# Performance work log

Hardware: AMD Instinct MI355X
Metric: run time of the kernel (lower is better)

Reference implementation:

```python
import jax, jax.numpy as jnp
import numpy as np

B, T, K, H, HID, OUT = 128, 128, 8, 3, 256, 2
LOG_STD_MIN, LOG_STD_MAX = -20.0, 2.0


def setup_inputs() -> dict:
    key = jax.random.key(0)
    ks = jax.random.split(key, 12)
    def lin(k, fan_in, fan_out, scale=0.05):
        return jax.random.normal(k, (fan_in, fan_out), dtype=jnp.float32) * scale
    return {
        "state": jax.random.normal(ks[0], (B, T, K), dtype=jnp.float32),
        "noise": jax.random.normal(ks[1], (B, T, OUT), dtype=jnp.float32),
        "Wq": lin(ks[2], K, H * K),
        "Wk": lin(ks[3], K, H * K),
        "Wv": lin(ks[4], K, H * K),
        "W1": lin(ks[5], H * K + K, HID),
        "b1": jnp.zeros((HID,), jnp.float32),
        "W2": lin(ks[6], HID, HID),
        "b2": jnp.zeros((HID,), jnp.float32),
        "Wmu": jax.random.uniform(ks[7], (HID, OUT), jnp.float32, -0.003, 0.003),
        "bmu": jax.random.uniform(ks[8], (OUT,), jnp.float32, -0.003, 0.003),
        "Wls": jax.random.uniform(ks[9], (HID, OUT), jnp.float32, -0.003, 0.003),
        "bls": jax.random.uniform(ks[10], (OUT,), jnp.float32, -0.003, 0.003),
    }


def reference(state, noise, Wq, Wk, Wv, W1, b1, W2, b2, Wmu, bmu, Wls, bls):
    b, t, k = state.shape
    h = H
    # off-diagonal gather indices: idx[i, m] = m if m < i else m + 1  (j != i, ascending)
    cols = jnp.arange(t - 1)
    idx = cols[None, :] + (cols[None, :] >= jnp.arange(t)[:, None]).astype(jnp.int32)  # [t, t-1]
    # rel_state[b, i, m] = state[b, idx[i, m]] - state[b, i]   -> [b, t, t-1, k]
    rel = state[:, idx, :] - state[:, :, None, :]
    # per-head projections (no bias)
    q = (state @ Wq).reshape(b, t, h, k)                      # [b, t, h, k]
    keys = (rel @ Wk).reshape(b, t, t - 1, h, k)              # [b, t, t-1, h, k]
    vals = (rel @ Wv).reshape(b, t, t - 1, h, k)
    # each query attends over its own t-1 relative keys
    scores = jnp.einsum("bthk,btmhk->bhtm", q, keys) / jnp.sqrt(jnp.float32(k))
    w = jax.nn.softmax(scores, axis=-1)                       # [b, h, t, t-1]
    x = jnp.einsum("bhtm,btmhk->bthk", w, vals).reshape(b, t, h * k)
    x = jnp.concatenate([x, state], axis=-1)                  # [b, t, h*k + k]
    x = jax.nn.relu(x @ W1 + b1)
    x = jax.nn.relu(x @ W2 + b2)
    mu = jnp.tanh(x @ Wmu + bmu)
    log_std = jnp.tanh(x @ Wls + bls)
    log_std = LOG_STD_MIN + 0.5 * (LOG_STD_MAX - LOG_STD_MIN) * (log_std + 1.0)
    std = jnp.exp(log_std)
    z = mu + std * noise                                      # rsample
    action = jnp.tanh(z)
    half_log_2pi = jnp.float32(0.5 * np.log(2.0 * np.pi))
    normal_lp = -0.5 * noise * noise - log_std - half_log_2pi
    log_prob = normal_lp - jnp.log(1.0 - action * action + 1e-7)
    log_prob = jnp.sum(log_prob, axis=-1, keepdims=True)
    return action, log_prob
```

## Files before the change

### kernel.cpp

```cpp
#include <hip/hip_runtime.h>
#include <math.h>

namespace {
constexpr int B_  = 128;
constexpr int T_  = 128;
constexpr int K_  = 8;
constexpr int H_  = 3;
constexpr int HK_ = 24;
constexpr int HID_ = 256;
constexpr int OUT_ = 2;
constexpr int AW_  = 32;
}

typedef __attribute__((ext_vector_type(8))) short bf16x8;
typedef __attribute__((ext_vector_type(4))) float f32x4;

__device__ inline unsigned short f2bf(float x) {
    unsigned int u = __float_as_uint(x);
    u += 0x7FFFu + ((u >> 16) & 1u);
    return (unsigned short)(u >> 16);
}
__device__ inline float bflo(unsigned int u) { return __uint_as_float(u << 16); }
__device__ inline float bfhi(unsigned int u) { return __uint_as_float(u & 0xFFFF0000u); }

__global__ __launch_bounds__(256) void prep_kernel(
    const float* __restrict__ W1, const float* __restrict__ W2,
    unsigned short* __restrict__ w1t, unsigned short* __restrict__ w2t)
{
    int idx = blockIdx.x * 256 + threadIdx.x;
    if (idx < 65536) {
        int k = idx >> 8, n = idx & 255;
        w2t[n * 256 + k] = f2bf(W2[idx]);
    } else {
        int r = idx - 65536;
        int k = r >> 8, n = r & 255;
        w1t[n * 32 + k] = f2bf(W1[r]);
    }
}

__global__ __launch_bounds__(256) void fused_actor_kernel(
    const float* __restrict__ state,
    const float* __restrict__ noise,
    const float* __restrict__ Wq, const float* __restrict__ Wk,
    const float* __restrict__ Wv,
    const unsigned short* __restrict__ w1t, const float* __restrict__ b1,
    const unsigned short* __restrict__ w2t, const float* __restrict__ b2,
    const float* __restrict__ Wmu, const float* __restrict__ bmu,
    const float* __restrict__ Wls, const float* __restrict__ bls,
    float* __restrict__ out)
{
    __shared__ alignas(16) float st[T_][K_];
    __shared__ float wq_s[K_*HK_], wk_s[K_*HK_], wv_s[K_*HK_];
    __shared__ alignas(16) float Qs[32][HK_];
    __shared__ alignas(16) unsigned short Kb[H_][T_][8];
    __shared__ alignas(16) unsigned short Vb[H_][T_][8];
    __shared__ alignas(16) unsigned short a0b[32][40];
    __shared__ alignas(16) unsigned short x1s[32][264];
    __shared__ alignas(16) float Whs[HID_][4];
    __shared__ alignas(16) float hp[4][32][4];

    const int tid = threadIdx.x;
    const int b   = blockIdx.x >> 2;
    const int iq  = blockIdx.x & 3;

    ((float4*)&st[0][0])[tid] = ((const float4*)(state + (size_t)b*T_*K_))[tid];
    if (tid < K_*HK_) { wq_s[tid]=Wq[tid]; wk_s[tid]=Wk[tid]; wv_s[tid]=Wv[tid]; }
    Whs[tid][0] = Wmu[tid*OUT_+0]; Whs[tid][1] = Wmu[tid*OUT_+1];
    Whs[tid][2] = Wls[tid*OUT_+0]; Whs[tid][3] = Wls[tid*OUT_+1];
    __syncthreads();

    #pragma unroll
    for (int it = 0; it < 12; ++it) {
        int idx = it*256 + tid;
        int j = idx / HK_, col = idx % HK_;
        int h = col >> 3, k = col & 7;
        float ak = 0.f, av = 0.f;
        #pragma unroll
        for (int m = 0; m < K_; ++m) {
            float sv = st[j][m];
            ak = fmaf(sv, wk_s[m*HK_+col], ak);
            av = fmaf(sv, wv_s[m*HK_+col], av);
        }
        Kb[h][j][k] = f2bf(ak);
        Vb[h][j][k] = f2bf(av);
    }
    #pragma unroll
    for (int it = 0; it < 3; ++it) {
        int idx = it*256 + tid;
        int il = idx / HK_, col = idx % HK_;
        float aq = 0.f;
        #pragma unroll
        for (int m = 0; m < K_; ++m)
            aq = fmaf(st[iq*32+il][m], wq_s[m*HK_+col], aq);
        Qs[il][col] = aq * 0.35355339059327373f;
    }
    __syncthreads();

    const int w    = tid >> 6;
    const int lane = tid & 63;

    {
        const int i_sub = lane >> 3, jg = lane & 7;
        #pragma unroll
        for (int p = 0; p < 3; ++p) {
            const int pair = w*3 + p;
            const int h  = pair >> 2;
            const int ig = pair & 3;
            const int il = ig*8 + i_sub;
            const int iglob = iq*32 + il;
            const float4 q0 = *(const float4*)&Qs[il][h*8];
            const float4 q1 = *(const float4*)&Qs[il][h*8+4];
            float l = 0.f;
            float acc[8] = {0.f,0.f,0.f,0.f,0.f,0.f,0.f,0.f};
            #pragma unroll 4
            for (int t = 0; t < 16; ++t) {
                const int j = t*8 + jg;
                const int4 kk = *(const int4*)&Kb[h][j][0];
                float s;
                s = q0.x * bflo(kk.x) + q0.y * bfhi(kk.x)
                  + q0.z * bflo(kk.y) + q0.w * bfhi(kk.y)
                  + q1.x * bflo(kk.z) + q1.y * bfhi(kk.z)
                  + q1.z * bflo(kk.w) + q1.w * bfhi(kk.w);
                const float e = (j == iglob) ? 0.f : __expf(s);
                l += e;
                const int4 vv = *(const int4*)&Vb[h][j][0];
                acc[0] = fmaf(e, bflo(vv.x), acc[0]);
                acc[1] = fmaf(e, bfhi(vv.x), acc[1]);
                acc[2] = fmaf(e, bflo(vv.y), acc[2]);
                acc[3] = fmaf(e, bfhi(vv.y), acc[3]);
                acc[4] = fmaf(e, bflo(vv.z), acc[4]);
                acc[5] = fmaf(e, bfhi(vv.z), acc[5]);
                acc[6] = fmaf(e, bflo(vv.w), acc[6]);
                acc[7] = fmaf(e, bfhi(vv.w), acc[7]);
            }
            #pragma unroll
            for (int off = 1; off <= 4; off <<= 1) {
                l += __shfl_xor(l, off, 64);
                #pragma unroll
                for (int k = 0; k < 8; ++k) acc[k] += __shfl_xor(acc[k], off, 64);
            }
            if (jg == 0) {
                const float rl = 1.f / l;
                const int4 vi = *(const int4*)&Vb[h][iglob][0];
                float vs[8] = { bflo(vi.x), bfhi(vi.x), bflo(vi.y), bfhi(vi.y),
                                bflo(vi.z), bfhi(vi.z), bflo(vi.w), bfhi(vi.w) };
                unsigned int r01 = (unsigned int)f2bf(acc[0]*rl - vs[0])
                                 | ((unsigned int)f2bf(acc[1]*rl - vs[1]) << 16);
                unsigned int r23 = (unsigned int)f2bf(acc[2]*rl - vs[2])
                                 | ((unsigned int)f2bf(acc[3]*rl - vs[3]) << 16);
                unsigned int r45 = (unsigned int)f2bf(acc[4]*rl - vs[4])
                                 | ((unsigned int)f2bf(acc[5]*rl - vs[5]) << 16);
                unsigned int r67 = (unsigned int)f2bf(acc[6]*rl - vs[6])
                                 | ((unsigned int)f2bf(acc[7]*rl - vs[7]) << 16);
                int4 rr; rr.x = r01; rr.y = r23; rr.z = r45; rr.w = r67;
                *(int4*)&a0b[il][h*8] = rr;
            }
        }
    }
    {
        int il = tid >> 3, k = tid & 7;
        a0b[il][HK_ + k] = f2bf(st[iq*32 + il][k]);
    }
    __syncthreads();

    const int lq = (tid >> 4) & 3;
    const int ln = tid & 15;

    {
        bf16x8 a0 = *(const bf16x8*)&a0b[ln][lq*8];
        bf16x8 a1 = *(const bf16x8*)&a0b[16+ln][lq*8];
        #pragma unroll
        for (int nt = 0; nt < 4; ++nt) {
            const int n0 = (w*4 + nt)*16;
            bf16x8 bf = *(const bf16x8*)(w1t + (size_t)(n0+ln)*32 + lq*8);
            const float bias = b1[n0+ln];
            f32x4 c = {bias, bias, bias, bias};
            f32x4 d0 = __builtin_amdgcn_mfma_f32_16x16x32_bf16(a0, bf, c, 0, 0, 0);
            f32x4 d1 = __builtin_amdgcn_mfma_f32_16x16x32_bf16(a1, bf, c, 0, 0, 0);
            #pragma unroll
            for (int r = 0; r < 4; ++r) {
                x1s[lq*4 + r][n0+ln]      = f2bf(fmaxf(d0[r], 0.f));
                x1s[16 + lq*4 + r][n0+ln] = f2bf(fmaxf(d1[r], 0.f));
            }
        }
    }
    __syncthreads();

    f32x4 acc2[2][4];
    #pragma unroll
    for (int nt = 0; nt < 4; ++nt) {
        const float bias = b2[(w*4+nt)*16 + ln];
        f32x4 c = {bias, bias, bias, bias};
        acc2[0][nt] = c; acc2[1][nt] = c;
    }
    #pragma unroll 2
    for (int ks = 0; ks < 8; ++ks) {
        const int k0 = ks*32;
        bf16x8 a0 = *(const bf16x8*)&x1s[ln][k0 + lq*8];
        bf16x8 a1 = *(const bf16x8*)&x1s[16+ln][k0 + lq*8];
        #pragma unroll
        for (int nt = 0; nt < 4; ++nt) {
            bf16x8 bf = *(const bf16x8*)(w2t + (size_t)((w*4+nt)*16+ln)*256 + k0 + lq*8);
            acc2[0][nt] = __builtin_amdgcn_mfma_f32_16x16x32_bf16(a0, bf, acc2[0][nt], 0,0,0);
            acc2[1][nt] = __builtin_amdgcn_mfma_f32_16x16x32_bf16(a1, bf, acc2[1][nt], 0,0,0);
        }
    }

    {
        float p[2][4][4];
        #pragma unroll
        for (int mt = 0; mt < 2; ++mt)
            #pragma unroll
            for (int r = 0; r < 4; ++r)
                #pragma unroll
                for (int o = 0; o < 4; ++o) p[mt][r][o] = 0.f;
        #pragma unroll
        for (int nt = 0; nt < 4; ++nt) {
            const int n = (w*4+nt)*16 + ln;
            const f32x4 wh = *(const f32x4*)&Whs[n][0];
            #pragma unroll
            for (int mt = 0; mt < 2; ++mt) {
                #pragma unroll
                for (int r = 0; r < 4; ++r) {
                    const float x2 = fmaxf(acc2[mt][nt][r], 0.f);
                    p[mt][r][0] = fmaf(x2, wh[0], p[mt][r][0]);
                    p[mt][r][1] = fmaf(x2, wh[1], p[mt][r][1]);
                    p[mt][r][2] = fmaf(x2, wh[2], p[mt][r][2]);
                    p[mt][r][3] = fmaf(x2, wh[3], p[mt][r][3]);
                }
            }
        }
        #pragma unroll
        for (int off = 1; off <= 8; off <<= 1)
            #pragma unroll
            for (int mt = 0; mt < 2; ++mt)
                #pragma unroll
                for (int r = 0; r < 4; ++r)
                    #pragma unroll
                    for (int o = 0; o < 4; ++o)
                        p[mt][r][o] += __shfl_xor(p[mt][r][o], off, 64);
        if (ln == 0) {
            #pragma unroll
            for (int mt = 0; mt < 2; ++mt)
                #pragma unroll
                for (int r = 0; r < 4; ++r) {
                    f32x4 pv = {p[mt][r][0], p[mt][r][1], p[mt][r][2], p[mt][r][3]};
                    *(f32x4*)&hp[w][mt*16 + lq*4 + r][0] = pv;
                }
        }
    }
    __syncthreads();

    if (tid < 32) {
        const int r = tid;
        const int grow = b*T_ + iq*32 + r;
        float pre[4];
        #pragma unroll
        for (int o = 0; o < 4; ++o)
            pre[o] = hp[0][r][o] + hp[1][r][o] + hp[2][r][o] + hp[3][r][o];
        float lp = 0.f;
        #pragma unroll
        for (int o = 0; o < OUT_; ++o) {
            float mu  = tanhf(pre[o]   + bmu[o]);
            float lsp = tanhf(pre[2+o] + bls[o]);
            float log_std = -20.f + 11.f * (lsp + 1.f);
            float sd = __expf(log_std);
            float n  = noise[(size_t)grow*OUT_ + o];
            float z  = fmaf(sd, n, mu);
            float a  = tanhf(z);
            out[(size_t)grow*OUT_ + o] = a;
            lp += -0.5f*n*n - log_std - 0.91893853320467274f
                  - logf(1.f - a*a + 1e-7f);
        }
        out[(size_t)B_*T_*OUT_ + grow] = lp;
    }
}

extern "C" void kernel_launch(void* const* d_in, const int* in_sizes, int n_in,
                              void* d_out, int out_size, void* d_ws, size_t ws_size,
                              hipStream_t stream)
{
    const float* state = (const float*)d_in[0];
    const float* noise = (const float*)d_in[1];
    const float* Wq  = (const float*)d_in[2];
    const float* Wk  = (const float*)d_in[3];
    const float* Wv  = (const float*)d_in[4];
    const float* W1  = (const float*)d_in[5];
    const float* b1  = (const float*)d_in[6];
    const float* W2  = (const float*)d_in[7];
    const float* b2  = (const float*)d_in[8];
    const float* Wmu = (const float*)d_in[9];
    const float* bmu = (const float*)d_in[10];
    const float* Wls = (const float*)d_in[11];
    const float* bls = (const float*)d_in[12];
    float* out = (float*)d_out;

    unsigned short* w1t = (unsigned short*)d_ws;
    unsigned short* w2t = w1t + 8192;

    prep_kernel<<<dim3(288), dim3(256), 0, stream>>>(W1, W2, w1t, w2t);
    fused_actor_kernel<<<dim3(B_*4), dim3(256), 0, stream>>>(
        state, noise, Wq, Wk, Wv, w1t, b1, w2t, b2, Wmu, bmu, Wls, bls, out);
}
```

Measured before the change: 101.7 us.

## Halve rows per block to double grid size and vectorize weight prep

Each block now handles 16 query rows instead of 32, so the grid doubles to 1024 blocks and the attention loop uses 16 lanes per row with shorter trip counts. The MLP stage keeps one MFMA row tile per wave. The K/V projection is restructured so each thread computes a full key row and writes it with a vector store. The prep kernel now writes packed 8-element bf16 vectors per thread. The trade-off is that K/V projection and weight loads are repeated across twice as many blocks.

```diff
diff --git a/kernel.cpp b/kernel.cpp
--- a/kernel.cpp
+++ b/kernel.cpp
@@ -9,7 +9,6 @@
 constexpr int HK_ = 24;
 constexpr int HID_ = 256;
 constexpr int OUT_ = 2;
-constexpr int AW_  = 32;
 }
 
 typedef __attribute__((ext_vector_type(8))) short bf16x8;
@@ -27,14 +26,18 @@
     const float* __restrict__ W1, const float* __restrict__ W2,
     unsigned short* __restrict__ w1t, unsigned short* __restrict__ w2t)
 {
-    int idx = blockIdx.x * 256 + threadIdx.x;
-    if (idx < 65536) {
-        int k = idx >> 8, n = idx & 255;
-        w2t[n * 256 + k] = f2bf(W2[idx]);
+    const int n = threadIdx.x;
+    unsigned short tmp[8];
+    if (blockIdx.x < 32) {
+        const int k0 = blockIdx.x * 8;
+        #pragma unroll
+        for (int i = 0; i < 8; ++i) tmp[i] = f2bf(W2[(size_t)(k0+i)*HID_ + n]);
+        *(bf16x8*)(w2t + (size_t)n*256 + k0) = *(const bf16x8*)tmp;
     } else {
-        int r = idx - 65536;
-        int k = r >> 8, n = r & 255;
-        w1t[n * 32 + k] = f2bf(W1[r]);
+        const int k0 = (blockIdx.x - 32) * 8;
+        #pragma unroll
+        for (int i = 0; i < 8; ++i) tmp[i] = f2bf(W1[(size_t)(k0+i)*HID_ + n]);
+        *(bf16x8*)(w1t + (size_t)n*32 + k0) = *(const bf16x8*)tmp;
     }
 }
 
@@ -51,48 +54,61 @@
 {
     __shared__ alignas(16) float st[T_][K_];
     __shared__ float wq_s[K_*HK_], wk_s[K_*HK_], wv_s[K_*HK_];
-    __shared__ alignas(16) float Qs[32][HK_];
+    __shared__ alignas(16) float Qs[16][HK_];
     __shared__ alignas(16) unsigned short Kb[H_][T_][8];
     __shared__ alignas(16) unsigned short Vb[H_][T_][8];
-    __shared__ alignas(16) unsigned short a0b[32][40];
-    __shared__ alignas(16) unsigned short x1s[32][264];
+    __shared__ alignas(16) unsigned short a0b[16][40];
+    __shared__ alignas(16) unsigned short x1s[16][264];
     __shared__ alignas(16) float Whs[HID_][4];
-    __shared__ alignas(16) float hp[4][32][4];
+    __shared__ alignas(16) float hp[4][16][4];
 
     const int tid = threadIdx.x;
-    const int b   = blockIdx.x >> 2;
-    const int iq  = blockIdx.x & 3;
+    const int b   = blockIdx.x >> 3;
+    const int iq  = blockIdx.x & 7;
 
     ((float4*)&st[0][0])[tid] = ((const float4*)(state + (size_t)b*T_*K_))[tid];
     if (tid < K_*HK_) { wq_s[tid]=Wq[tid]; wk_s[tid]=Wk[tid]; wv_s[tid]=Wv[tid]; }
-    Whs[tid][0] = Wmu[tid*OUT_+0]; Whs[tid][1] = Wmu[tid*OUT_+1];
-    Whs[tid][2] = Wls[tid*OUT_+0]; Whs[tid][3] = Wls[tid*OUT_+1];
-    __syncthreads();
-
-    #pragma unroll
-    for (int it = 0; it < 12; ++it) {
-        int idx = it*256 + tid;
-        int j = idx / HK_, col = idx % HK_;
-        int h = col >> 3, k = col & 7;
-        float ak = 0.f, av = 0.f;
-        #pragma unroll
-        for (int m = 0; m < K_; ++m) {
-            float sv = st[j][m];
-            ak = fmaf(sv, wk_s[m*HK_+col], ak);
-            av = fmaf(sv, wv_s[m*HK_+col], av);
-        }
-        Kb[h][j][k] = f2bf(ak);
-        Vb[h][j][k] = f2bf(av);
-    }
-    #pragma unroll
-    for (int it = 0; it < 3; ++it) {
-        int idx = it*256 + tid;
-        int il = idx / HK_, col = idx % HK_;
-        float aq = 0.f;
-        #pragma unroll
-        for (int m = 0; m < K_; ++m)
-            aq = fmaf(st[iq*32+il][m], wq_s[m*HK_+col], aq);
-        Qs[il][col] = aq * 0.35355339059327373f;
+    { f32x4 wh = { Wmu[tid*OUT_+0], Wmu[tid*OUT_+1], Wls[tid*OUT_+0], Wls[tid*OUT_+1] };
+      *(f32x4*)&Whs[tid][0] = wh; }
+    __syncthreads();
+
+    if (tid < 128) {
+        const int j = tid;
+        const float4 s0 = *(const float4*)(state + (size_t)b*T_*K_ + j*8);
+        const float4 s1 = *(const float4*)(state + (size_t)b*T_*K_ + j*8 + 4);
+        const float sv[8] = {s0.x,s0.y,s0.z,s0.w,s1.x,s1.y,s1.z,s1.w};
+        #pragma unroll
+        for (int h = 0; h < H_; ++h) {
+            unsigned short kp[8], vp[8];
+            #pragma unroll
+            for (int k = 0; k < 8; ++k) {
+                const int col = h*8 + k;
+                float ak = 0.f, av = 0.f;
+                #pragma unroll
+                for (int m = 0; m < K_; ++m) {
+                    ak = fmaf(sv[m], wk_s[m*HK_+col], ak);
+                    av = fmaf(sv[m], wv_s[m*HK_+col], av);
+                }
+                kp[k] = f2bf(ak); vp[k] = f2bf(av);
+            }
+            *(bf16x8*)&Kb[h][j][0] = *(const bf16x8*)kp;
+            *(bf16x8*)&Vb[h][j][0] = *(const bf16x8*)vp;
+        }
+    } else {
+        const int t2 = tid - 128;
+        const int il = t2 >> 3;
+        const int c0 = (t2 & 7) * 3;
+        const float4 s0 = *(const float4*)&st[iq*16 + il][0];
+        const float4 s1 = *(const float4*)&st[iq*16 + il][4];
+        const float sv[8] = {s0.x,s0.y,s0.z,s0.w,s1.x,s1.y,s1.z,s1.w};
+        #pragma unroll
+        for (int cc = 0; cc < 3; ++cc) {
+            const int col = c0 + cc;
+            float aq = 0.f;
+            #pragma unroll
+            for (int m = 0; m < K_; ++m) aq = fmaf(sv[m], wq_s[m*HK_+col], aq);
+            Qs[il][col] = aq * 0.35355339059327373f;
+        }
     }
     __syncthreads();
 
@@ -100,21 +116,21 @@
     const int lane = tid & 63;
 
     {
-        const int i_sub = lane >> 3, jg = lane & 7;
+        const int i_sub = lane >> 4, jg = lane & 15;
         #pragma unroll
         for (int p = 0; p < 3; ++p) {
-            const int pair = w*3 + p;
-            const int h  = pair >> 2;
-            const int ig = pair & 3;
-            const int il = ig*8 + i_sub;
-            const int iglob = iq*32 + il;
+            const int pp = w*3 + p;
+            const int h  = pp >> 2;
+            const int ig = pp & 3;
+            const int il = ig*4 + i_sub;
+            const int iglob = iq*16 + il;
             const float4 q0 = *(const float4*)&Qs[il][h*8];
             const float4 q1 = *(const float4*)&Qs[il][h*8+4];
             float l = 0.f;
             float acc[8] = {0.f,0.f,0.f,0.f,0.f,0.f,0.f,0.f};
-            #pragma unroll 4
-            for (int t = 0; t < 16; ++t) {
-                const int j = t*8 + jg;
+            #pragma unroll
+            for (int t = 0; t < 8; ++t) {
+                const int j = t*16 + jg;
                 const int4 kk = *(const int4*)&Kb[h][j][0];
                 float s;
                 s = q0.x * bflo(kk.x) + q0.y * bfhi(kk.x)
@@ -134,7 +150,7 @@
                 acc[7] = fmaf(e, bfhi(vv.w), acc[7]);
             }
             #pragma unroll
-            for (int off = 1; off <= 4; off <<= 1) {
+            for (int off = 1; off <= 8; off <<= 1) {
                 l += __shfl_xor(l, off, 64);
                 #pragma unroll
                 for (int k = 0; k < 8; ++k) acc[k] += __shfl_xor(acc[k], off, 64);
@@ -142,8 +158,8 @@
             if (jg == 0) {
                 const float rl = 1.f / l;
                 const int4 vi = *(const int4*)&Vb[h][iglob][0];
-                float vs[8] = { bflo(vi.x), bfhi(vi.x), bflo(vi.y), bfhi(vi.y),
-                                bflo(vi.z), bfhi(vi.z), bflo(vi.w), bfhi(vi.w) };
+                const float vs[8] = { bflo(vi.x), bfhi(vi.x), bflo(vi.y), bfhi(vi.y),
+                                      bflo(vi.z), bfhi(vi.z), bflo(vi.w), bfhi(vi.w) };
                 unsigned int r01 = (unsigned int)f2bf(acc[0]*rl - vs[0])
                                  | ((unsigned int)f2bf(acc[1]*rl - vs[1]) << 16);
                 unsigned int r23 = (unsigned int)f2bf(acc[2]*rl - vs[2])
@@ -157,9 +173,9 @@
             }
         }
     }
-    {
-        int il = tid >> 3, k = tid & 7;
-        a0b[il][HK_ + k] = f2bf(st[iq*32 + il][k]);
+    if (tid < 128) {
+        const int il = tid >> 3, k = tid & 7;
+        a0b[il][HK_ + k] = f2bf(st[iq*16 + il][k]);
     }
     __syncthreads();
 
@@ -167,93 +183,78 @@
     const int ln = tid & 15;
 
     {
-        bf16x8 a0 = *(const bf16x8*)&a0b[ln][lq*8];
-        bf16x8 a1 = *(const bf16x8*)&a0b[16+ln][lq*8];
+        const bf16x8 a0 = *(const bf16x8*)&a0b[ln][lq*8];
         #pragma unroll
         for (int nt = 0; nt < 4; ++nt) {
             const int n0 = (w*4 + nt)*16;
-            bf16x8 bf = *(const bf16x8*)(w1t + (size_t)(n0+ln)*32 + lq*8);
+            const bf16x8 bf = *(const bf16x8*)(w1t + (size_t)(n0+ln)*32 + lq*8);
             const float bias = b1[n0+ln];
             f32x4 c = {bias, bias, bias, bias};
-            f32x4 d0 = __builtin_amdgcn_mfma_f32_16x16x32_bf16(a0, bf, c, 0, 0, 0);
-            f32x4 d1 = __builtin_amdgcn_mfma_f32_16x16x32_bf16(a1, bf, c, 0, 0, 0);
-            #pragma unroll
-            for (int r = 0; r < 4; ++r) {
-                x1s[lq*4 + r][n0+ln]      = f2bf(fmaxf(d0[r], 0.f));
-                x1s[16 + lq*4 + r][n0+ln] = f2bf(fmaxf(d1[r], 0.f));
-            }
-        }
-    }
-    __syncthreads();
-
-    f32x4 acc2[2][4];
+            f32x4 d = __builtin_amdgcn_mfma_f32_16x16x32_bf16(a0, bf, c, 0, 0, 0);
+            #pragma unroll
+            for (int r = 0; r < 4; ++r)
+                x1s[lq*4 + r][n0+ln] = f2bf(fmaxf(d[r], 0.f));
+        }
+    }
+    __syncthreads();
+
+    f32x4 acc2[4];
     #pragma unroll
     for (int nt = 0; nt < 4; ++nt) {
         const float bias = b2[(w*4+nt)*16 + ln];
         f32x4 c = {bias, bias, bias, bias};
-        acc2[0][nt] = c; acc2[1][nt] = c;
+        acc2[nt] = c;
     }
     #pragma unroll 2
     for (int ks = 0; ks < 8; ++ks) {
         const int k0 = ks*32;
-        bf16x8 a0 = *(const bf16x8*)&x1s[ln][k0 + lq*8];
-        bf16x8 a1 = *(const bf16x8*)&x1s[16+ln][k0 + lq*8];
+        const bf16x8 a0 = *(const bf16x8*)&x1s[ln][k0 + lq*8];
         #pragma unroll
         for (int nt = 0; nt < 4; ++nt) {
-            bf16x8 bf = *(const bf16x8*)(w2t + (size_t)((w*4+nt)*16+ln)*256 + k0 + lq*8);
-            acc2[0][nt] = __builtin_amdgcn_mfma_f32_16x16x32_bf16(a0, bf, acc2[0][nt], 0,0,0);
-            acc2[1][nt] = __builtin_amdgcn_mfma_f32_16x16x32_bf16(a1, bf, acc2[1][nt], 0,0,0);
+            const bf16x8 bf = *(const bf16x8*)(w2t + (size_t)((w*4+nt)*16+ln)*256 + k0 + lq*8);
+            acc2[nt] = __builtin_amdgcn_mfma_f32_16x16x32_bf16(a0, bf, acc2[nt], 0, 0, 0);
         }
     }
 
     {
-        float p[2][4][4];
-        #pragma unroll
-        for (int mt = 0; mt < 2; ++mt)
-            #pragma unroll
-            for (int r = 0; r < 4; ++r)
-                #pragma unroll
-                for (int o = 0; o < 4; ++o) p[mt][r][o] = 0.f;
+        float p[4][4];
+        #pragma unroll
+        for (int r = 0; r < 4; ++r)
+            #pragma unroll
+            for (int o = 0; o < 4; ++o) p[r][o] = 0.f;
         #pragma unroll
         for (int nt = 0; nt < 4; ++nt) {
             const int n = (w*4+nt)*16 + ln;
             const f32x4 wh = *(const f32x4*)&Whs[n][0];
             #pragma unroll
-            for (int mt = 0; mt < 2; ++mt) {
+            for (int r = 0; r < 4; ++r) {
+                const float x2 = fmaxf(acc2[nt][r], 0.f);
+                p[r][0] = fmaf(x2, wh[0], p[r][0]);
+                p[r][1] = fmaf(x2, wh[1], p[r][1]);
+                p[r][2] = fmaf(x2, wh[2], p[r][2]);
+                p[r][3] = fmaf(x2, wh[3], p[r][3]);
+            }
+        }
+        #pragma unroll
+        for (int off = 1; off <= 8; off <<= 1)
+            #pragma unroll
+            for (int r = 0; r < 4; ++r)
                 #pragma unroll
-                for (int r = 0; r < 4; ++r) {
-                    const float x2 = fmaxf(acc2[mt][nt][r], 0.f);
-                    p[mt][r][0] = fmaf(x2, wh[0], p[mt][r][0]);
-                    p[mt][r][1] = fmaf(x2, wh[1], p[mt][r][1]);
-                    p[mt][r][2] = fmaf(x2, wh[2], p[mt][r][2]);
-                    p[mt][r][3] = fmaf(x2, wh[3], p[mt][r][3]);
-                }
-            }
-        }
-        #pragma unroll
-        for (int off = 1; off <= 8; off <<= 1)
-            #pragma unroll
-            for (int mt = 0; mt < 2; ++mt)
-                #pragma unroll
-                for (int r = 0; r < 4; ++r)
-                    #pragma unroll
-                    for (int o = 0; o < 4; ++o)
-                        p[mt][r][o] += __shfl_xor(p[mt][r][o], off, 64);
+                for (int o = 0; o < 4; ++o)
+                    p[r][o] += __shfl_xor(p[r][o], off, 64);
         if (ln == 0) {
             #pragma unroll
-            for (int mt = 0; mt < 2; ++mt)
-                #pragma unroll
-                for (int r = 0; r < 4; ++r) {
-                    f32x4 pv = {p[mt][r][0], p[mt][r][1], p[mt][r][2], p[mt][r][3]};
-                    *(f32x4*)&hp[w][mt*16 + lq*4 + r][0] = pv;
-                }
-        }
-    }
-    __syncthreads();
-
-    if (tid < 32) {
+            for (int r = 0; r < 4; ++r) {
+                f32x4 pv = {p[r][0], p[r][1], p[r][2], p[r][3]};
+                *(f32x4*)&hp[w][lq*4 + r][0] = pv;
+            }
+        }
+    }
+    __syncthreads();
+
+    if (tid < 16) {
         const int r = tid;
-        const int grow = b*T_ + iq*32 + r;
+        const int grow = b*T_ + iq*16 + r;
         float pre[4];
         #pragma unroll
         for (int o = 0; o < 4; ++o)
@@ -298,7 +299,7 @@
     unsigned short* w1t = (unsigned short*)d_ws;
     unsigned short* w2t = w1t + 8192;
 
-    prep_kernel<<<dim3(288), dim3(256), 0, stream>>>(W1, W2, w1t, w2t);
-    fused_actor_kernel<<<dim3(B_*4), dim3(256), 0, stream>>>(
+    prep_kernel<<<dim3(36), dim3(256), 0, stream>>>(W1, W2, w1t, w2t);
+    fused_actor_kernel<<<dim3(B_*8), dim3(256), 0, stream>>>(
         state, noise, Wq, Wk, Wv, w1t, b1, w2t, b2, Wmu, bmu, Wls, bls, out);
 }
```

Measured after the change: 111.5 us. +9.7%, slower.

## Precompute Q/K/V projections once per batch in prep kernel and use DPP reductions

Applied to the files above, without the earlier changes.

Moves the K/V/Q projections out of the fused kernel into the prep kernel, so they are computed once per batch instead of once per quarter-block (4x redundant before). The results are stored to global workspace in bf16/fp32, and the attention loop reads them from global/L2 rather than LDS. Cross-lane shuffle reductions are replaced by DPP-based adds, and the prep kernel's weight transposes now use vectorized stores. The risk is extra global traffic and the attention inner loop hitting L2 instead of LDS.

```diff
diff --git a/kernel.cpp b/kernel.cpp
--- a/kernel.cpp
+++ b/kernel.cpp
@@ -9,7 +9,6 @@
 constexpr int HK_ = 24;
 constexpr int HID_ = 256;
 constexpr int OUT_ = 2;
-constexpr int AW_  = 32;
 }
 
 typedef __attribute__((ext_vector_type(8))) short bf16x8;
@@ -23,79 +22,115 @@
 __device__ inline float bflo(unsigned int u) { return __uint_as_float(u << 16); }
 __device__ inline float bfhi(unsigned int u) { return __uint_as_float(u & 0xFFFF0000u); }
 
+template <int CTRL>
+__device__ inline float dpp_add(float v) {
+    int t = __builtin_amdgcn_update_dpp(0, __float_as_int(v), CTRL, 0xF, 0xF, true);
+    return v + __int_as_float(t);
+}
+__device__ inline float red8(float v) {
+    v = dpp_add<0xB1>(v); v = dpp_add<0x4E>(v); return dpp_add<0x141>(v);
+}
+__device__ inline float red16(float v) {
+    return dpp_add<0x140>(red8(v));
+}
+
 __global__ __launch_bounds__(256) void prep_kernel(
+    const float* __restrict__ state,
+    const float* __restrict__ Wq, const float* __restrict__ Wk,
+    const float* __restrict__ Wv,
     const float* __restrict__ W1, const float* __restrict__ W2,
-    unsigned short* __restrict__ w1t, unsigned short* __restrict__ w2t)
+    unsigned short* __restrict__ w1t, unsigned short* __restrict__ w2t,
+    unsigned short* __restrict__ kb, unsigned short* __restrict__ vb,
+    float* __restrict__ qsc)
 {
-    int idx = blockIdx.x * 256 + threadIdx.x;
-    if (idx < 65536) {
-        int k = idx >> 8, n = idx & 255;
-        w2t[n * 256 + k] = f2bf(W2[idx]);
+    __shared__ float wq_s[K_*HK_], wk_s[K_*HK_], wv_s[K_*HK_];
+    const int tid = threadIdx.x;
+    const int blk = blockIdx.x;
+
+    if (blk < 32) {
+        const int k0 = blk * 8;
+        unsigned short tmp[8];
+        #pragma unroll
+        for (int i = 0; i < 8; ++i) tmp[i] = f2bf(W2[(size_t)(k0+i)*HID_ + tid]);
+        *(bf16x8*)(w2t + (size_t)tid*256 + k0) = *(const bf16x8*)tmp;
+        return;
+    }
+    if (blk < 36) {
+        const int k0 = (blk - 32) * 8;
+        unsigned short tmp[8];
+        #pragma unroll
+        for (int i = 0; i < 8; ++i) tmp[i] = f2bf(W1[(size_t)(k0+i)*HID_ + tid]);
+        *(bf16x8*)(w1t + (size_t)tid*32 + k0) = *(const bf16x8*)tmp;
+        return;
+    }
+
+    const int b = blk - 36;
+    if (tid < K_*HK_) { wq_s[tid]=Wq[tid]; wk_s[tid]=Wk[tid]; wv_s[tid]=Wv[tid]; }
+    __syncthreads();
+
+    const float* sb = state + (size_t)b*T_*K_;
+    if (tid < 128) {
+        const int j = tid;
+        const float4 s0 = *(const float4*)(sb + j*8);
+        const float4 s1 = *(const float4*)(sb + j*8 + 4);
+        const float sv[8] = {s0.x,s0.y,s0.z,s0.w,s1.x,s1.y,s1.z,s1.w};
+        #pragma unroll
+        for (int h = 0; h < H_; ++h) {
+            unsigned short kp[8], vp[8];
+            #pragma unroll
+            for (int k = 0; k < 8; ++k) {
+                const int col = h*8 + k;
+                float ak = 0.f, av = 0.f;
+                #pragma unroll
+                for (int m = 0; m < K_; ++m) {
+                    ak = fmaf(sv[m], wk_s[m*HK_+col], ak);
+                    av = fmaf(sv[m], wv_s[m*HK_+col], av);
+                }
+                kp[k] = f2bf(ak); vp[k] = f2bf(av);
+            }
+            const size_t off = ((size_t)(b*H_ + h)*T_ + j) * 8;
+            *(bf16x8*)(kb + off) = *(const bf16x8*)kp;
+            *(bf16x8*)(vb + off) = *(const bf16x8*)vp;
+        }
     } else {
-        int r = idx - 65536;
-        int k = r >> 8, n = r & 255;
-        w1t[n * 32 + k] = f2bf(W1[r]);
+        const int i = tid - 128;
+        const float4 s0 = *(const float4*)(sb + i*8);
+        const float4 s1 = *(const float4*)(sb + i*8 + 4);
+        const float sv[8] = {s0.x,s0.y,s0.z,s0.w,s1.x,s1.y,s1.z,s1.w};
+        float q[HK_];
+        #pragma unroll
+        for (int col = 0; col < HK_; ++col) {
+            float aq = 0.f;
+            #pragma unroll
+            for (int m = 0; m < K_; ++m) aq = fmaf(sv[m], wq_s[m*HK_+col], aq);
+            q[col] = aq * 0.35355339059327373f;
+        }
+        float* qo = qsc + (size_t)(b*T_ + i)*HK_;
+        #pragma unroll
+        for (int c = 0; c < 6; ++c)
+            *(float4*)(qo + c*4) = *(const float4*)&q[c*4];
     }
 }
 
 __global__ __launch_bounds__(256) void fused_actor_kernel(
     const float* __restrict__ state,
     const float* __restrict__ noise,
-    const float* __restrict__ Wq, const float* __restrict__ Wk,
-    const float* __restrict__ Wv,
+    const unsigned short* __restrict__ kb, const unsigned short* __restrict__ vb,
+    const float* __restrict__ qsc,
     const unsigned short* __restrict__ w1t, const float* __restrict__ b1,
     const unsigned short* __restrict__ w2t, const float* __restrict__ b2,
     const float* __restrict__ Wmu, const float* __restrict__ bmu,
     const float* __restrict__ Wls, const float* __restrict__ bls,
     float* __restrict__ out)
 {
-    __shared__ alignas(16) float st[T_][K_];
-    __shared__ float wq_s[K_*HK_], wk_s[K_*HK_], wv_s[K_*HK_];
-    __shared__ alignas(16) float Qs[32][HK_];
-    __shared__ alignas(16) unsigned short Kb[H_][T_][8];
-    __shared__ alignas(16) unsigned short Vb[H_][T_][8];
     __shared__ alignas(16) unsigned short a0b[32][40];
     __shared__ alignas(16) unsigned short x1s[32][264];
-    __shared__ alignas(16) float Whs[HID_][4];
     __shared__ alignas(16) float hp[4][32][4];
 
-    const int tid = threadIdx.x;
-    const int b   = blockIdx.x >> 2;
-    const int iq  = blockIdx.x & 3;
-
-    ((float4*)&st[0][0])[tid] = ((const float4*)(state + (size_t)b*T_*K_))[tid];
-    if (tid < K_*HK_) { wq_s[tid]=Wq[tid]; wk_s[tid]=Wk[tid]; wv_s[tid]=Wv[tid]; }
-    Whs[tid][0] = Wmu[tid*OUT_+0]; Whs[tid][1] = Wmu[tid*OUT_+1];
-    Whs[tid][2] = Wls[tid*OUT_+0]; Whs[tid][3] = Wls[tid*OUT_+1];
-    __syncthreads();
-
-    #pragma unroll
-    for (int it = 0; it < 12; ++it) {
-        int idx = it*256 + tid;
-        int j = idx / HK_, col = idx % HK_;
-        int h = col >> 3, k = col & 7;
-        float ak = 0.f, av = 0.f;
-        #pragma unroll
-        for (int m = 0; m < K_; ++m) {
-            float sv = st[j][m];
-            ak = fmaf(sv, wk_s[m*HK_+col], ak);
-            av = fmaf(sv, wv_s[m*HK_+col], av);
-        }
-        Kb[h][j][k] = f2bf(ak);
-        Vb[h][j][k] = f2bf(av);
-    }
-    #pragma unroll
-    for (int it = 0; it < 3; ++it) {
-        int idx = it*256 + tid;
-        int il = idx / HK_, col = idx % HK_;
-        float aq = 0.f;
-        #pragma unroll
-        for (int m = 0; m < K_; ++m)
-            aq = fmaf(st[iq*32+il][m], wq_s[m*HK_+col], aq);
-        Qs[il][col] = aq * 0.35355339059327373f;
-    }
-    __syncthreads();
-
+    const int tid  = threadIdx.x;
+    const int b    = blockIdx.x >> 2;
+    const int iq   = blockIdx.x & 3;
+    const int i0   = iq * 32;
     const int w    = tid >> 6;
     const int lane = tid & 63;
 
@@ -107,15 +142,18 @@
             const int h  = pair >> 2;
             const int ig = pair & 3;
             const int il = ig*8 + i_sub;
-            const int iglob = iq*32 + il;
-            const float4 q0 = *(const float4*)&Qs[il][h*8];
-            const float4 q1 = *(const float4*)&Qs[il][h*8+4];
+            const int iglob = i0 + il;
+            const float* qp = qsc + (size_t)(b*T_ + iglob)*HK_ + h*8;
+            const float4 q0 = *(const float4*)qp;
+            const float4 q1 = *(const float4*)(qp + 4);
+            const unsigned short* kbase = kb + (size_t)(b*H_ + h)*T_*8;
+            const unsigned short* vbase = vb + (size_t)(b*H_ + h)*T_*8;
             float l = 0.f;
             float acc[8] = {0.f,0.f,0.f,0.f,0.f,0.f,0.f,0.f};
             #pragma unroll 4
             for (int t = 0; t < 16; ++t) {
                 const int j = t*8 + jg;
-                const int4 kk = *(const int4*)&Kb[h][j][0];
+                const int4 kk = *(const int4*)(kbase + j*8);
                 float s;
                 s = q0.x * bflo(kk.x) + q0.y * bfhi(kk.x)
                   + q0.z * bflo(kk.y) + q0.w * bfhi(kk.y)
@@ -123,7 +161,7 @@
                   + q1.z * bflo(kk.w) + q1.w * bfhi(kk.w);
                 const float e = (j == iglob) ? 0.f : __expf(s);
                 l += e;
-                const int4 vv = *(const int4*)&Vb[h][j][0];
+                const int4 vv = *(const int4*)(vbase + j*8);
                 acc[0] = fmaf(e, bflo(vv.x), acc[0]);
                 acc[1] = fmaf(e, bfhi(vv.x), acc[1]);
                 acc[2] = fmaf(e, bflo(vv.y), acc[2]);
@@ -133,17 +171,14 @@
                 acc[6] = fmaf(e, bflo(vv.w), acc[6]);
                 acc[7] = fmaf(e, bfhi(vv.w), acc[7]);
             }
-            #pragma unroll
-            for (int off = 1; off <= 4; off <<= 1) {
-                l += __shfl_xor(l, off, 64);
-                #pragma unroll
-                for (int k = 0; k < 8; ++k) acc[k] += __shfl_xor(acc[k], off, 64);
-            }
+            l = red8(l);
+            #pragma unroll
+            for (int k = 0; k < 8; ++k) acc[k] = red8(acc[k]);
             if (jg == 0) {
                 const float rl = 1.f / l;
-                const int4 vi = *(const int4*)&Vb[h][iglob][0];
-                float vs[8] = { bflo(vi.x), bfhi(vi.x), bflo(vi.y), bfhi(vi.y),
-                                bflo(vi.z), bfhi(vi.z), bflo(vi.w), bfhi(vi.w) };
+                const int4 vi = *(const int4*)(vbase + iglob*8);
+                const float vs[8] = { bflo(vi.x), bfhi(vi.x), bflo(vi.y), bfhi(vi.y),
+                                      bflo(vi.z), bfhi(vi.z), bflo(vi.w), bfhi(vi.w) };
                 unsigned int r01 = (unsigned int)f2bf(acc[0]*rl - vs[0])
                                  | ((unsigned int)f2bf(acc[1]*rl - vs[1]) << 16);
                 unsigned int r23 = (unsigned int)f2bf(acc[2]*rl - vs[2])
@@ -158,8 +193,8 @@
         }
     }
     {
-        int il = tid >> 3, k = tid & 7;
-        a0b[il][HK_ + k] = f2bf(st[iq*32 + il][k]);
+        const int il = tid >> 3, k = tid & 7;
+        a0b[il][HK_ + k] = f2bf(state[(size_t)b*T_*K_ + (i0 + il)*K_ + k]);
     }
     __syncthreads();
 
@@ -167,12 +202,12 @@
     const int ln = tid & 15;
 
     {
-        bf16x8 a0 = *(const bf16x8*)&a0b[ln][lq*8];
-        bf16x8 a1 = *(const bf16x8*)&a0b[16+ln][lq*8];
+        const bf16x8 a0 = *(const bf16x8*)&a0b[ln][lq*8];
+        const bf16x8 a1 = *(const bf16x8*)&a0b[16+ln][lq*8];
         #pragma unroll
         for (int nt = 0; nt < 4; ++nt) {
             const int n0 = (w*4 + nt)*16;
-            bf16x8 bf = *(const bf16x8*)(w1t + (size_t)(n0+ln)*32 + lq*8);
+            const bf16x8 bf = *(const bf16x8*)(w1t + (size_t)(n0+ln)*32 + lq*8);
             const float bias = b1[n0+ln];
             f32x4 c = {bias, bias, bias, bias};
             f32x4 d0 = __builtin_amdgcn_mfma_f32_16x16x32_bf16(a0, bf, c, 0, 0, 0);
@@ -196,11 +231,11 @@
     #pragma unroll 2
     for (int ks = 0; ks < 8; ++ks) {
         const int k0 = ks*32;
-        bf16x8 a0 = *(const bf16x8*)&x1s[ln][k0 + lq*8];
-        bf16x8 a1 = *(const bf16x8*)&x1s[16+ln][k0 + lq*8];
+        const bf16x8 a0 = *(const bf16x8*)&x1s[ln][k0 + lq*8];
+        const bf16x8 a1 = *(const bf16x8*)&x1s[16+ln][k0 + lq*8];
         #pragma unroll
         for (int nt = 0; nt < 4; ++nt) {
-            bf16x8 bf = *(const bf16x8*)(w2t + (size_t)((w*4+nt)*16+ln)*256 + k0 + lq*8);
+            const bf16x8 bf = *(const bf16x8*)(w2t + (size_t)((w*4+nt)*16+ln)*256 + k0 + lq*8);
             acc2[0][nt] = __builtin_amdgcn_mfma_f32_16x16x32_bf16(a0, bf, acc2[0][nt], 0,0,0);
             acc2[1][nt] = __builtin_amdgcn_mfma_f32_16x16x32_bf16(a1, bf, acc2[1][nt], 0,0,0);
         }
@@ -217,28 +252,27 @@
         #pragma unroll
         for (int nt = 0; nt < 4; ++nt) {
             const int n = (w*4+nt)*16 + ln;
-            const f32x4 wh = *(const f32x4*)&Whs[n][0];
+            const float2 wm = *(const float2*)(Wmu + n*OUT_);
+            const float2 wl = *(const float2*)(Wls + n*OUT_);
             #pragma unroll
             for (int mt = 0; mt < 2; ++mt) {
                 #pragma unroll
                 for (int r = 0; r < 4; ++r) {
                     const float x2 = fmaxf(acc2[mt][nt][r], 0.f);
-                    p[mt][r][0] = fmaf(x2, wh[0], p[mt][r][0]);
-                    p[mt][r][1] = fmaf(x2, wh[1], p[mt][r][1]);
-                    p[mt][r][2] = fmaf(x2, wh[2], p[mt][r][2]);
-                    p[mt][r][3] = fmaf(x2, wh[3], p[mt][r][3]);
+                    p[mt][r][0] = fmaf(x2, wm.x, p[mt][r][0]);
+                    p[mt][r][1] = fmaf(x2, wm.y, p[mt][r][1]);
+                    p[mt][r][2] = fmaf(x2, wl.x, p[mt][r][2]);
+                    p[mt][r][3] = fmaf(x2, wl.y, p[mt][r][3]);
                 }
             }
         }
         #pragma unroll
-        for (int off = 1; off <= 8; off <<= 1)
-            #pragma unroll
-            for (int mt = 0; mt < 2; ++mt)
-                #pragma unroll
-                for (int r = 0; r < 4; ++r)
-                    #pragma unroll
-                    for (int o = 0; o < 4; ++o)
-                        p[mt][r][o] += __shfl_xor(p[mt][r][o], off, 64);
+        for (int mt = 0; mt < 2; ++mt)
+            #pragma unroll
+            for (int r = 0; r < 4; ++r)
+                #pragma unroll
+                for (int o = 0; o < 4; ++o)
+                    p[mt][r][o] = red16(p[mt][r][o]);
         if (ln == 0) {
             #pragma unroll
             for (int mt = 0; mt < 2; ++mt)
@@ -253,7 +287,7 @@
 
     if (tid < 32) {
         const int r = tid;
-        const int grow = b*T_ + iq*32 + r;
+        const int grow = b*T_ + i0 + r;
         float pre[4];
         #pragma unroll
         for (int o = 0; o < 4; ++o)
@@ -297,8 +331,12 @@
 
     unsigned short* w1t = (unsigned short*)d_ws;
     unsigned short* w2t = w1t + 8192;
-
-    prep_kernel<<<dim3(288), dim3(256), 0, stream>>>(W1, W2, w1t, w2t);
+    unsigned short* kbp = w2t + 65536;
+    unsigned short* vbp = kbp + 393216;
+    float*          qsp = (float*)(vbp + 393216);
+
+    prep_kernel<<<dim3(164), dim3(256), 0, stream>>>(
+        state, Wq, Wk, Wv, W1, W2, w1t, w2t, kbp, vbp, qsp);
     fused_actor_kernel<<<dim3(B_*4), dim3(256), 0, stream>>>(
-        state, noise, Wq, Wk, Wv, w1t, b1, w2t, b2, Wmu, bmu, Wls, bls, out);
-}
+        state, noise, kbp, vbp, qsp, w1t, b1, w2t, b2, Wmu, bmu, Wls, bls, out);
+}
```

Measured after the change: 106.9 us. +5.2%, slower.
